# Optimization experiments

Measured on AMD Instinct MI355X. Metric: run time of the kernel, lower is better.

The kernel has to match this reference:

```python
import jax, jax.numpy as jnp
import numpy as np

N_NODES = 50000
HEADS = 4
OUT_DIM = 64
NEG_SLOPE = 0.2
BETA = 0.5
C_CONST = 1.0
EPS = 1e-16


def setup_inputs() -> dict:
    key = jax.random.key(0)
    ks = jax.random.split(key, 6)
    in_dim = 128
    x = jax.random.normal(ks[0], (N_NODES, in_dim), dtype=jnp.float32)
    edge_index = jax.random.randint(ks[1], (2, 800000), 0, N_NODES, dtype=jnp.int64)
    # GATConv params (glorot-ish scale)
    W = jax.random.normal(ks[2], (in_dim, HEADS * OUT_DIM), dtype=jnp.float32) * (1.0 / np.sqrt(in_dim))
    att_src = jax.random.normal(ks[3], (HEADS, OUT_DIM), dtype=jnp.float32) * (1.0 / np.sqrt(OUT_DIM))
    att_dst = jax.random.normal(ks[4], (HEADS, OUT_DIM), dtype=jnp.float32) * (1.0 / np.sqrt(OUT_DIM))
    bias = jnp.zeros((HEADS * OUT_DIM,), dtype=jnp.float32)
    return {"x": x, "edge_index": edge_index, "W": W, "att_src": att_src,
            "att_dst": att_dst, "bias": bias}


def _gat_conv(x, edge_index, W, att_src, att_dst, bias):
    N = x.shape[0]
    # add self loops (PyG GATConv default)
    loop = jnp.arange(N, dtype=edge_index.dtype)
    src = jnp.concatenate([edge_index[0], loop])
    dst = jnp.concatenate([edge_index[1], loop])
    # linear transform: [N, H, F]
    h = (x @ W).reshape(N, HEADS, OUT_DIM)
    # per-node attention logits: [N, H]
    a_src = jnp.einsum('nhf,hf->nh', h, att_src)
    a_dst = jnp.einsum('nhf,hf->nh', h, att_dst)
    # per-edge logits and segment softmax over destination nodes
    e = jax.nn.leaky_relu(a_src[src] + a_dst[dst], negative_slope=NEG_SLOPE)  # [E, H]
    m = jax.ops.segment_max(e, dst, num_segments=N)                           # [N, H]
    ex = jnp.exp(e - m[dst])
    s = jax.ops.segment_sum(ex, dst, num_segments=N)                          # [N, H]
    alpha = ex / (s[dst] + EPS)                                               # [E, H]
    # aggregate messages: [N, H, F]
    out = jax.ops.segment_sum(alpha[:, :, None] * h[src], dst, num_segments=N)
    return out.reshape(N, HEADS * OUT_DIM) + bias


def reference(x, edge_index, W, att_src, att_dst, bias):
    # eval mode: feature dropout and attention dropout are identity
    z = _gat_conv(x, edge_index, W, att_src, att_dst, bias)
    return BETA * z + (C_CONST - BETA) * jax.nn.elu(z)
```

## Files before the change

kernel.cpp:

```cpp
#include <hip/hip_runtime.h>
#include <hip/hip_bf16.h>

typedef unsigned short u16;
typedef __attribute__((ext_vector_type(8))) short bf16x8;
typedef __attribute__((ext_vector_type(4))) float f32x4;

#define HEADS 4
#define OUT_DIM 64
#define HF 256
#define IN_DIM 128
#define NEG_SLOPE 0.2f
#define EPSF 1e-16f

__device__ __forceinline__ float braw2f(u16 u) {
    union { float f; unsigned int i; } c; c.i = ((unsigned int)u) << 16; return c.f;
}
__device__ __forceinline__ u16 f2braw(float v) {
    __hip_bfloat16 t = __float2bfloat16(v);
    return *(u16*)&t;
}
__device__ __forceinline__ float lrelu(float e) { return e < 0.f ? NEG_SLOPE * e : e; }

__device__ __forceinline__ bool detect_i64(const int* ei) {
    return (ei[1] | ei[3] | ei[5] | ei[7] | ei[9] | ei[11] | ei[13] | ei[15]) == 0;
}
__device__ __forceinline__ void get_edge(const int* ei, int E, int t, bool i64,
                                         int& s, int& d) {
    if (t < E) {
        if (i64) { s = ei[2 * t]; d = ei[2 * (E + t)]; }
        else     { s = ei[t];     d = ei[E + t]; }
    } else {
        s = d = t - E;
    }
}

__global__ __launch_bounds__(256) void init_kernel(const float* __restrict__ W,
                                                   const float* __restrict__ att_s,
                                                   const float* __restrict__ att_d,
                                                   float* __restrict__ wa_s,
                                                   float* __restrict__ wa_d,
                                                   int* __restrict__ cnt,
                                                   int* __restrict__ cur,
                                                   int* __restrict__ gcnt,
                                                   int* __restrict__ hist,
                                                   int* __restrict__ bcur,
                                                   int N, int NZ) {
    int b = blockIdx.x;
    if (b == 0) {
        if (threadIdx.x == 0) *gcnt = 0;
        hist[threadIdx.x] = 0;
        bcur[threadIdx.x] = 0;
    }
    if (b < NZ) {
        int i = b * 256 + threadIdx.x;
        if (i < N) { cnt[i] = 0; cur[i] = 0; }
    } else {
        for (int idx = threadIdx.x; idx < HEADS * IN_DIM; idx += 256) {
            int h = idx >> 7, k = idx & 127;
            float ss = 0.f, sd = 0.f;
            for (int f = 0; f < OUT_DIM; ++f) {
                float wv = W[k * HF + h * OUT_DIM + f];
                ss = fmaf(wv, att_s[h * OUT_DIM + f], ss);
                sd = fmaf(wv, att_d[h * OUT_DIM + f], sd);
            }
            wa_s[idx] = ss;
            wa_d[idx] = sd;
        }
    }
}

__global__ __launch_bounds__(256) void phase1_kernel(const float* __restrict__ x,
                                                     const int* __restrict__ ei,
                                                     const float* __restrict__ W,
                                                     const float* __restrict__ wa_s,
                                                     const float* __restrict__ wa_d,
                                                     float* __restrict__ a_src,
                                                     float* __restrict__ a_dst,
                                                     u16* __restrict__ xb,
                                                     u16* __restrict__ Wfrag,
                                                     int* __restrict__ cnt,
                                                     int N, int E, int NA, int NC) {
    int b = blockIdx.x;
    if (b < NA) {
        int wid = threadIdx.x >> 6;
        int l = threadIdx.x & 63;
        int g = l >> 4, c = l & 15, kc = c * 8;
        int v = b * 16 + wid * 4 + g;
        if (v >= N) return;

        const float4* xr = (const float4*)(x + (size_t)v * IN_DIM + kc);
        float4 x0 = xr[0], x1 = xr[1];

        uint4 u;
        u.x = (unsigned)f2braw(x0.x) | ((unsigned)f2braw(x0.y) << 16);
        u.y = (unsigned)f2braw(x0.z) | ((unsigned)f2braw(x0.w) << 16);
        u.z = (unsigned)f2braw(x1.x) | ((unsigned)f2braw(x1.y) << 16);
        u.w = (unsigned)f2braw(x1.z) | ((unsigned)f2braw(x1.w) << 16);
        *(uint4*)(xb + (size_t)v * IN_DIM + kc) = u;

        float ps[4], pd[4];
        #pragma unroll
        for (int h = 0; h < 4; ++h) {
            const float4* s4 = (const float4*)(wa_s + h * IN_DIM + kc);
            const float4* d4 = (const float4*)(wa_d + h * IN_DIM + kc);
            float4 s0 = s4[0], s1 = s4[1], d0 = d4[0], d1 = d4[1];
            ps[h] = x0.x*s0.x + x0.y*s0.y + x0.z*s0.z + x0.w*s0.w
                  + x1.x*s1.x + x1.y*s1.y + x1.z*s1.z + x1.w*s1.w;
            pd[h] = x0.x*d0.x + x0.y*d0.y + x0.z*d0.z + x0.w*d0.w
                  + x1.x*d1.x + x1.y*d1.y + x1.z*d1.z + x1.w*d1.w;
        }
        #pragma unroll
        for (int off = 1; off < 16; off <<= 1) {
            #pragma unroll
            for (int h = 0; h < 4; ++h) {
                ps[h] += __shfl_xor(ps[h], off);
                pd[h] += __shfl_xor(pd[h], off);
            }
        }
        if (c == 0) {
            float4 vs, vd;
            vs.x = ps[0]; vs.y = ps[1]; vs.z = ps[2]; vs.w = ps[3];
            vd.x = pd[0]; vd.y = pd[1]; vd.z = pd[2]; vd.w = pd[3];
            *(float4*)(a_src + (size_t)v * HEADS) = vs;
            *(float4*)(a_dst + (size_t)v * HEADS) = vd;
        }
    } else if (b < NA + NC) {
        int t = (b - NA) * 256 + threadIdx.x;
        if (t >= E + N) return;
        bool i64 = detect_i64(ei);
        int src, dst; get_edge(ei, E, t, i64, src, dst);
        if (src >= 0 && src < N && dst >= 0 && dst < N) atomicAdd(cnt + dst, 1);
    } else {
        int bb = b - NA - NC;
        for (int idx = bb * 256 + threadIdx.x; idx < 32768; idx += 8 * 256) {
            int j = idx & 7, l = (idx >> 3) & 63, t = (idx >> 9) & 3;
            int s = (idx >> 11) & 3, h = (idx >> 13) & 3;
            int k = s * 32 + ((l >> 4) & 3) * 8 + j;
            int col = h * OUT_DIM + t * 16 + (l & 15);
            Wfrag[idx] = f2braw(W[k * HF + col]);
        }
    }
}

__global__ __launch_bounds__(256) void offset_kernel(const int* __restrict__ cnt,
                                                     int* __restrict__ offs,
                                                     int* __restrict__ gcnt,
                                                     int* __restrict__ hist, int N) {
    __shared__ int lh[256];
    lh[threadIdx.x] = 0;
    __syncthreads();

    int idx = blockIdx.x * 256 + threadIdx.x;
    int l = threadIdx.x & 63;
    int d = (idx < N) ? cnt[idx] : 0;
    if (idx < N) atomicAdd(lh + min(max(d, 0), 255), 1);

    int s = d;
    #pragma unroll
    for (int off = 1; off < 64; off <<= 1) {
        int t = __shfl_up(s, off);
        if (l >= off) s += t;
    }
    int base = 0;
    if (l == 63) base = atomicAdd(gcnt, s);
    base = __shfl(base, 63);
    if (idx < N) offs[idx] = base + s - d;

    __syncthreads();
    if (lh[threadIdx.x]) atomicAdd(hist + threadIdx.x, lh[threadIdx.x]);
}

__global__ __launch_bounds__(256) void bscan_kernel(const int* __restrict__ hist,
                                                    int* __restrict__ bbase, int N) {
    __shared__ int sc[256];
    int tid = threadIdx.x;
    sc[tid] = hist[tid];
    __syncthreads();
    #pragma unroll
    for (int off = 1; off < 256; off <<= 1) {
        int t = (tid >= off) ? sc[tid - off] : 0;
        __syncthreads();
        sc[tid] += t;
        __syncthreads();
    }
    bbase[tid] = N - sc[tid];
}

__global__ __launch_bounds__(256) void scatter_kernel(const int* __restrict__ cnt,
                                                      const int* __restrict__ bbase,
                                                      int* __restrict__ bcur,
                                                      int* __restrict__ perm, int N) {
    __shared__ int lh[256];
    __shared__ int lbase[256];
    lh[threadIdx.x] = 0;
    __syncthreads();

    int idx = blockIdx.x * 256 + threadIdx.x;
    int b = 0, mypos = 0;
    bool valid = (idx < N);
    if (valid) {
        b = min(max(cnt[idx], 0), 255);
        mypos = atomicAdd(lh + b, 1);
    }
    __syncthreads();
    int c = lh[threadIdx.x];
    if (c) lbase[threadIdx.x] = atomicAdd(bcur + threadIdx.x, c);
    __syncthreads();
    if (valid) {
        int p = bbase[b] + lbase[b] + mypos;
        if (p >= 0 && p < N) perm[p] = idx;
    }
}

__global__ __launch_bounds__(256) void fill_kernel(const int* __restrict__ ei,
                                                   const int* __restrict__ offs,
                                                   int* __restrict__ cur,
                                                   int* __restrict__ slots,
                                                   uint2* __restrict__ wslots,
                                                   const float* __restrict__ a_src,
                                                   const float* __restrict__ a_dst,
                                                   int E, int N) {
    int t = blockIdx.x * 256 + threadIdx.x;
    if (t >= E + N) return;
    bool i64 = detect_i64(ei);
    int src, dst; get_edge(ei, E, t, i64, src, dst);
    if (src >= 0 && src < N && dst >= 0 && dst < N) {
        int pos = atomicAdd(cur + dst, 1);
        int idx = offs[dst] + pos;
        slots[idx] = src;
        if (wslots) {
            float4 as = ((const float4*)a_src)[src];
            float4 ad = ((const float4*)a_dst)[dst];
            float w0 = __expf(lrelu(as.x + ad.x));
            float w1 = __expf(lrelu(as.y + ad.y));
            float w2 = __expf(lrelu(as.z + ad.z));
            float w3 = __expf(lrelu(as.w + ad.w));
            uint2 wp;
            wp.x = (unsigned)f2braw(w0) | ((unsigned)f2braw(w1) << 16);
            wp.y = (unsigned)f2braw(w2) | ((unsigned)f2braw(w3) << 16);
            wslots[idx] = wp;
        }
    }
}

#define ACC_EDGE(wp, r) do { \
    float w0_ = braw2f((wp).x & 0xffff), w1_ = braw2f((wp).x >> 16); \
    float w2_ = braw2f((wp).y & 0xffff), w3_ = braw2f((wp).y >> 16); \
    ls0 += w0_; ls1 += w1_; ls2 += w2_; ls3 += w3_; \
    float xv_[8]; \
    xv_[0] = braw2f((r).x & 0xffff); xv_[1] = braw2f((r).x >> 16); \
    xv_[2] = braw2f((r).y & 0xffff); xv_[3] = braw2f((r).y >> 16); \
    xv_[4] = braw2f((r).z & 0xffff); xv_[5] = braw2f((r).z >> 16); \
    xv_[6] = braw2f((r).w & 0xffff); xv_[7] = braw2f((r).w >> 16); \
    _Pragma("unroll") \
    for (int q_ = 0; q_ < 8; ++q_) { \
        G0[q_] = fmaf(w0_, xv_[q_], G0[q_]); \
        G1[q_] = fmaf(w1_, xv_[q_], G1[q_]); \
        G2[q_] = fmaf(w2_, xv_[q_], G2[q_]); \
        G3[q_] = fmaf(w3_, xv_[q_], G3[q_]); \
    } \
} while (0)

__global__ __launch_bounds__(512) void fused_gz_kernel(const int* __restrict__ perm,
                                                       const int* __restrict__ offs,
                                                       const int* __restrict__ cnt,
                                                       const int* __restrict__ slots,
                                                       const uint2* __restrict__ wslots,
                                                       const u16* __restrict__ xb,
                                                       const u16* __restrict__ Wfrag,
                                                       const float* __restrict__ bias,
                                                       float* __restrict__ out,
                                                       int N, int ET) {
    __shared__ u16 smem[32 * 520];
    __shared__ int pvals[32];

    int tid = threadIdx.x;
    int wid = tid >> 6;
    int l = tid & 63;
    int g = l >> 4, c = l & 15, kc = c * 8;
    int n = wid * 4 + g;
    int pidx = blockIdx.x * 32 + n;

    int v = -1;
    if (pidx < N) {
        v = perm[pidx];
        if (v < 0 || v >= N) v = -1;
    }
    if (c == 0) pvals[n] = v;

    int beg = 0, end = 0;
    if (v >= 0) {
        beg = offs[v];
        int deg = cnt[v];
        beg = max(0, min(beg, ET));
        end = max(beg, min(beg + deg, ET));
    }

    float ls0 = 0.f, ls1 = 0.f, ls2 = 0.f, ls3 = 0.f;
    float G0[8] = {0,0,0,0,0,0,0,0};
    float G1[8] = {0,0,0,0,0,0,0,0};
    float G2[8] = {0,0,0,0,0,0,0,0};
    float G3[8] = {0,0,0,0,0,0,0,0};

    int j = beg;
    for (; j + 4 <= end; j += 4) {
        int s0 = max(0, min(slots[j],     N - 1));
        int s1 = max(0, min(slots[j + 1], N - 1));
        int s2 = max(0, min(slots[j + 2], N - 1));
        int s3 = max(0, min(slots[j + 3], N - 1));
        uint2 wp0 = wslots[j];
        uint2 wp1 = wslots[j + 1];
        uint2 wp2 = wslots[j + 2];
        uint2 wp3 = wslots[j + 3];
        uint4 r0 = *(const uint4*)(xb + (size_t)s0 * IN_DIM + kc);
        uint4 r1 = *(const uint4*)(xb + (size_t)s1 * IN_DIM + kc);
        uint4 r2 = *(const uint4*)(xb + (size_t)s2 * IN_DIM + kc);
        uint4 r3 = *(const uint4*)(xb + (size_t)s3 * IN_DIM + kc);
        ACC_EDGE(wp0, r0);
        ACC_EDGE(wp1, r1);
        ACC_EDGE(wp2, r2);
        ACC_EDGE(wp3, r3);
    }
    for (; j < end; ++j) {
        int s0 = max(0, min(slots[j], N - 1));
        uint2 wp0 = wslots[j];
        uint4 r0 = *(const uint4*)(xb + (size_t)s0 * IN_DIM + kc);
        ACC_EDGE(wp0, r0);
    }

    if (v >= 0) {
        float i0 = 1.f / (ls0 + EPSF), i1 = 1.f / (ls1 + EPSF);
        float i2 = 1.f / (ls2 + EPSF), i3 = 1.f / (ls3 + EPSF);
        u16* lp = smem + n * 520 + c * 8;
        #pragma unroll
        for (int h = 0; h < 4; ++h) {
            const float* G = h == 0 ? G0 : h == 1 ? G1 : h == 2 ? G2 : G3;
            float inv = h == 0 ? i0 : h == 1 ? i1 : h == 2 ? i2 : i3;
            uint4 u;
            u.x = (unsigned)f2braw(G[0] * inv) | ((unsigned)f2braw(G[1] * inv) << 16);
            u.y = (unsigned)f2braw(G[2] * inv) | ((unsigned)f2braw(G[3] * inv) << 16);
            u.z = (unsigned)f2braw(G[4] * inv) | ((unsigned)f2braw(G[5] * inv) << 16);
            u.w = (unsigned)f2braw(G[6] * inv) | ((unsigned)f2braw(G[7] * inv) << 16);
            *(uint4*)(lp + h * 128) = u;
        }
    }
    __syncthreads();

    int t = wid >> 2;
    int h = wid & 3;
    int q = l >> 4, mcol = l & 15;

    const u16* lp = smem + (t * 16 + mcol) * 520 + h * 128 + q * 8;
    bf16x8 A[4];
    A[0] = *(const bf16x8*)(lp);
    A[1] = *(const bf16x8*)(lp + 32);
    A[2] = *(const bf16x8*)(lp + 64);
    A[3] = *(const bf16x8*)(lp + 96);

    f32x4 acc0 = {0.f,0.f,0.f,0.f}, acc1 = acc0, acc2 = acc0, acc3 = acc0;
    #pragma unroll
    for (int s = 0; s < 4; ++s) {
        const u16* wb = Wfrag + (((h * 4 + s) * 4) << 9) + l * 8;
        bf16x8 B0 = *(const bf16x8*)(wb);
        bf16x8 B1 = *(const bf16x8*)(wb + 512);
        bf16x8 B2 = *(const bf16x8*)(wb + 1024);
        bf16x8 B3 = *(const bf16x8*)(wb + 1536);
        acc0 = __builtin_amdgcn_mfma_f32_16x16x32_bf16(A[s], B0, acc0, 0, 0, 0);
        acc1 = __builtin_amdgcn_mfma_f32_16x16x32_bf16(A[s], B1, acc1, 0, 0, 0);
        acc2 = __builtin_amdgcn_mfma_f32_16x16x32_bf16(A[s], B2, acc2, 0, 0, 0);
        acc3 = __builtin_amdgcn_mfma_f32_16x16x32_bf16(A[s], B3, acc3, 0, 0, 0);
    }

    #pragma unroll
    for (int bt = 0; bt < 4; ++bt) {
        f32x4 a = bt == 0 ? acc0 : bt == 1 ? acc1 : bt == 2 ? acc2 : acc3;
        float b = bias[h * OUT_DIM + bt * 16 + mcol];
        #pragma unroll
        for (int r = 0; r < 4; ++r) {
            int vv = pvals[t * 16 + q * 4 + r];
            if (vv >= 0) {
                float z = a[r] + b;
                float y = z > 0.f ? z : 0.5f * z + 0.5f * (__expf(z) - 1.f);
                out[(size_t)vv * HF + h * OUT_DIM + bt * 16 + mcol] = y;
            }
        }
    }
}

__global__ __launch_bounds__(512) void gather_bf_kernel(const int* __restrict__ offs,
                                                        const int* __restrict__ cnt,
                                                        const int* __restrict__ slots,
                                                        const u16* __restrict__ xb,
                                                        const float* __restrict__ a_src,
                                                        const float* __restrict__ a_dst,
                                                        u16* __restrict__ Gout, int N, int ET) {
    int v = (blockIdx.x * 512 + threadIdx.x) >> 6;
    int l = threadIdx.x & 63;
    if (v >= N) return;
    int h = l >> 4, c = l & 15, kc = c * 8;

    int beg = offs[v];
    int deg = cnt[v];
    beg = max(0, min(beg, ET));
    int end = max(beg, min(beg + deg, ET));
    float adh = a_dst[v * HEADS + h];

    float ls = 0.f;
    float G[8] = {0.f,0.f,0.f,0.f,0.f,0.f,0.f,0.f};

    int j = beg;
    for (; j + 4 <= end; j += 4) {
        int s0 = max(0, min(slots[j],     N - 1));
        int s1 = max(0, min(slots[j + 1], N - 1));
        int s2 = max(0, min(slots[j + 2], N - 1));
        int s3 = max(0, min(slots[j + 3], N - 1));
        float w0 = __expf(lrelu(a_src[s0 * HEADS + h] + adh));
        float w1 = __expf(lrelu(a_src[s1 * HEADS + h] + adh));
        float w2 = __expf(lrelu(a_src[s2 * HEADS + h] + adh));
        float w3 = __expf(lrelu(a_src[s3 * HEADS + h] + adh));
        uint4 r0 = *(const uint4*)(xb + (size_t)s0 * IN_DIM + kc);
        uint4 r1 = *(const uint4*)(xb + (size_t)s1 * IN_DIM + kc);
        uint4 r2 = *(const uint4*)(xb + (size_t)s2 * IN_DIM + kc);
        uint4 r3 = *(const uint4*)(xb + (size_t)s3 * IN_DIM + kc);
        ls += (w0 + w1) + (w2 + w3);
        unsigned ua[4];
        ua[0]=r0.x; ua[1]=r0.y; ua[2]=r0.z; ua[3]=r0.w;
        #pragma unroll
        for (int q = 0; q < 4; ++q) {
            G[2*q]   = fmaf(w0, braw2f(ua[q] & 0xffff), G[2*q]);
            G[2*q+1] = fmaf(w0, braw2f(ua[q] >> 16),    G[2*q+1]);
        }
        ua[0]=r1.x; ua[1]=r1.y; ua[2]=r1.z; ua[3]=r1.w;
        #pragma unroll
        for (int q = 0; q < 4; ++q) {
            G[2*q]   = fmaf(w1, braw2f(ua[q] & 0xffff), G[2*q]);
            G[2*q+1] = fmaf(w1, braw2f(ua[q] >> 16),    G[2*q+1]);
        }
        ua[0]=r2.x; ua[1]=r2.y; ua[2]=r2.z; ua[3]=r2.w;
        #pragma unroll
        for (int q = 0; q < 4; ++q) {
            G[2*q]   = fmaf(w2, braw2f(ua[q] & 0xffff), G[2*q]);
            G[2*q+1] = fmaf(w2, braw2f(ua[q] >> 16),    G[2*q+1]);
        }
        ua[0]=r3.x; ua[1]=r3.y; ua[2]=r3.z; ua[3]=r3.w;
        #pragma unroll
        for (int q = 0; q < 4; ++q) {
            G[2*q]   = fmaf(w3, braw2f(ua[q] & 0xffff), G[2*q]);
            G[2*q+1] = fmaf(w3, braw2f(ua[q] >> 16),    G[2*q+1]);
        }
    }
    for (; j < end; ++j) {
        int s0 = max(0, min(slots[j], N - 1));
        float w0 = __expf(lrelu(a_src[s0 * HEADS + h] + adh));
        uint4 r0 = *(const uint4*)(xb + (size_t)s0 * IN_DIM + kc);
        ls += w0;
        unsigned ua[4]; ua[0]=r0.x; ua[1]=r0.y; ua[2]=r0.z; ua[3]=r0.w;
        #pragma unroll
        for (int q = 0; q < 4; ++q) {
            G[2*q]   = fmaf(w0, braw2f(ua[q] & 0xffff), G[2*q]);
            G[2*q+1] = fmaf(w0, braw2f(ua[q] >> 16),    G[2*q+1]);
        }
    }

    float inv = 1.f / (ls + EPSF);
    uint4 u;
    u.x = (unsigned)f2braw(G[0] * inv) | ((unsigned)f2braw(G[1] * inv) << 16);
    u.y = (unsigned)f2braw(G[2] * inv) | ((unsigned)f2braw(G[3] * inv) << 16);
    u.z = (unsigned)f2braw(G[4] * inv) | ((unsigned)f2braw(G[5] * inv) << 16);
    u.w = (unsigned)f2braw(G[6] * inv) | ((unsigned)f2braw(G[7] * inv) << 16);
    *(uint4*)(Gout + (size_t)v * 512 + h * 128 + kc) = u;
}

__global__ __launch_bounds__(512) void gather_f32_kernel(const int* __restrict__ offs,
                                                         const int* __restrict__ cnt,
                                                         const int* __restrict__ slots,
                                                         const float* __restrict__ x,
                                                         const float* __restrict__ a_src,
                                                         const float* __restrict__ a_dst,
                                                         u16* __restrict__ Gout, int N, int ET) {
    int v = (blockIdx.x * 512 + threadIdx.x) >> 6;
    int l = threadIdx.x & 63;
    if (v >= N) return;
    int h = l >> 4, c = l & 15, kc = c * 8;

    int beg = offs[v];
    int deg = cnt[v];
    beg = max(0, min(beg, ET));
    int end = max(beg, min(beg + deg, ET));
    float adh = a_dst[v * HEADS + h];

    float ls = 0.f;
    float G[8] = {0.f,0.f,0.f,0.f,0.f,0.f,0.f,0.f};
    for (int j = beg; j < end; ++j) {
        int s0 = max(0, min(slots[j], N - 1));
        float w0 = __expf(lrelu(a_src[s0 * HEADS + h] + adh));
        const float4* xr0 = (const float4*)(x + (size_t)s0 * IN_DIM + kc);
        float4 a0 = xr0[0], b0 = xr0[1];
        ls += w0;
        G[0]=fmaf(w0,a0.x,G[0]); G[1]=fmaf(w0,a0.y,G[1]);
        G[2]=fmaf(w0,a0.z,G[2]); G[3]=fmaf(w0,a0.w,G[3]);
        G[4]=fmaf(w0,b0.x,G[4]); G[5]=fmaf(w0,b0.y,G[5]);
        G[6]=fmaf(w0,b0.z,G[6]); G[7]=fmaf(w0,b0.w,G[7]);
    }
    float inv = 1.f / (ls + EPSF);
    uint4 u;
    u.x = (unsigned)f2braw(G[0] * inv) | ((unsigned)f2braw(G[1] * inv) << 16);
    u.y = (unsigned)f2braw(G[2] * inv) | ((unsigned)f2braw(G[3] * inv) << 16);
    u.z = (unsigned)f2braw(G[4] * inv) | ((unsigned)f2braw(G[5] * inv) << 16);
    u.w = (unsigned)f2braw(G[6] * inv) | ((unsigned)f2braw(G[7] * inv) << 16);
    *(uint4*)(Gout + (size_t)v * 512 + h * 128 + kc) = u;
}

__global__ __launch_bounds__(256) void zgemm_kernel(const u16* __restrict__ Wfrag,
                                                    const float* __restrict__ bias,
                                                    float* __restrict__ out, int N) {
    int h = threadIdx.x >> 6;
    int l = threadIdx.x & 63;
    int q = l >> 4, mcol = l & 15;
    int nb = blockIdx.x * 16;

    const u16* G = (const u16*)out;
    bool valid = (nb + mcol) < N;
    int vA = valid ? nb + mcol : N - 1;
    const u16* gp = G + (size_t)vA * 512 + h * 128 + q * 8;
    bf16x8 A[4];
    A[0] = *(const bf16x8*)(gp);
    A[1] = *(const bf16x8*)(gp + 32);
    A[2] = *(const bf16x8*)(gp + 64);
    A[3] = *(const bf16x8*)(gp + 96);
    if (!valid) {
        bf16x8 zz = {0,0,0,0,0,0,0,0};
        A[0] = zz; A[1] = zz; A[2] = zz; A[3] = zz;
    }

    f32x4 acc0 = {0.f,0.f,0.f,0.f}, acc1 = acc0, acc2 = acc0, acc3 = acc0;
    #pragma unroll
    for (int s = 0; s < 4; ++s) {
        const u16* wb = Wfrag + (((h * 4 + s) * 4) << 9) + l * 8;
        bf16x8 B0 = *(const bf16x8*)(wb);
        bf16x8 B1 = *(const bf16x8*)(wb + 512);
        bf16x8 B2 = *(const bf16x8*)(wb + 1024);
        bf16x8 B3 = *(const bf16x8*)(wb + 1536);
        acc0 = __builtin_amdgcn_mfma_f32_16x16x32_bf16(A[s], B0, acc0, 0, 0, 0);
        acc1 = __builtin_amdgcn_mfma_f32_16x16x32_bf16(A[s], B1, acc1, 0, 0, 0);
        acc2 = __builtin_amdgcn_mfma_f32_16x16x32_bf16(A[s], B2, acc2, 0, 0, 0);
        acc3 = __builtin_amdgcn_mfma_f32_16x16x32_bf16(A[s], B3, acc3, 0, 0, 0);
    }

    #pragma unroll
    for (int t = 0; t < 4; ++t) {
        f32x4 a = t == 0 ? acc0 : t == 1 ? acc1 : t == 2 ? acc2 : acc3;
        float b = bias[h * OUT_DIM + t * 16 + mcol];
        #pragma unroll
        for (int r = 0; r < 4; ++r) {
            int v = nb + q * 4 + r;
            if (v < N) {
                float z = a[r] + b;
                float y = z > 0.f ? z : 0.5f * z + 0.5f * (__expf(z) - 1.f);
                out[(size_t)v * HF + h * OUT_DIM + t * 16 + mcol] = y;
            }
        }
    }
}

extern "C" void kernel_launch(void* const* d_in, const int* in_sizes, int n_in,
                              void* d_out, int out_size, void* d_ws, size_t ws_size,
                              hipStream_t stream) {
    const float* x       = (const float*)d_in[0];
    const int*   ei      = (const int*)d_in[1];
    const float* W       = (const float*)d_in[2];
    const float* att_src = (const float*)d_in[3];
    const float* att_dst = (const float*)d_in[4];
    const float* bias    = (const float*)d_in[5];

    const int N = in_sizes[0] / IN_DIM;
    const int E = in_sizes[1] / 2;
    const int ET = E + N;
    const int NT = (N + 255) / 256;

    char* ws = (char*)d_ws;
    size_t off = 0;
    float* wa_s   = (float*)(ws + off); off += HEADS * IN_DIM * 4;
    float* wa_d   = (float*)(ws + off); off += HEADS * IN_DIM * 4;
    u16*   Wfrag  = (u16*)(ws + off);   off += 32768 * 2;
    float* a_src  = (float*)(ws + off); off += (size_t)N * HEADS * 4;
    float* a_dst  = (float*)(ws + off); off += (size_t)N * HEADS * 4;
    int*   offs   = (int*)(ws + off);   off += ((size_t)N * 4 + 15) & ~(size_t)15;
    int*   cnt    = (int*)(ws + off);   off += ((size_t)N * 4 + 15) & ~(size_t)15;
    int*   cur    = (int*)(ws + off);   off += ((size_t)N * 4 + 15) & ~(size_t)15;
    int*   gcnt   = (int*)(ws + off);   off += 64;
    int*   hist   = (int*)(ws + off);   off += 256 * 4;
    int*   bbase  = (int*)(ws + off);   off += 256 * 4;
    int*   bcur   = (int*)(ws + off);   off += 256 * 4;
    int*   perm   = (int*)(ws + off);   off += ((size_t)N * 4 + 15) & ~(size_t)15;
    int*   slots  = (int*)(ws + off);   off += ((size_t)ET * 4 + 15) & ~(size_t)15;
    u16*   xb     = (u16*)(ws + off);   size_t need_bf = off + (size_t)N * IN_DIM * 2;
    uint2* wslots = (uint2*)(ws + need_bf);
    size_t need_w = need_bf + (size_t)ET * 8;
    bool use_bf = (ws_size >= need_bf);
    bool use_w  = (ws_size >= need_w);

    const int NA = (N + 15) / 16;
    const int NC = (ET + 255) / 256;

    init_kernel<<<NT + 1, 256, 0, stream>>>(W, att_src, att_dst, wa_s, wa_d,
                                            cnt, cur, gcnt, hist, bcur, N, NT);
    phase1_kernel<<<NA + NC + 8, 256, 0, stream>>>(x, ei, W, wa_s, wa_d, a_src, a_dst,
                                                   use_bf ? xb : (u16*)d_out,
                                                   Wfrag, cnt, N, E, NA, NC);
    offset_kernel<<<NT, 256, 0, stream>>>(cnt, offs, gcnt, hist, N);
    fill_kernel<<<(ET + 255) / 256, 256, 0, stream>>>(ei, offs, cur, slots,
                                                      use_w ? wslots : (uint2*)0,
                                                      a_src, a_dst, E, N);
    if (use_w) {
        bscan_kernel<<<1, 256, 0, stream>>>(hist, bbase, N);
        scatter_kernel<<<NT, 256, 0, stream>>>(cnt, bbase, bcur, perm, N);
        fused_gz_kernel<<<(N + 31) / 32, 512, 0, stream>>>(perm, offs, cnt, slots,
                                                           wslots, xb, Wfrag, bias,
                                                           (float*)d_out, N, ET);
    } else if (use_bf) {
        gather_bf_kernel<<<(N * 64 + 511) / 512, 512, 0, stream>>>(offs, cnt, slots, xb,
                                                                   a_src, a_dst,
                                                                   (u16*)d_out, N, ET);
        zgemm_kernel<<<(N + 15) / 16, 256, 0, stream>>>(Wfrag, bias, (float*)d_out, N);
    } else {
        gather_f32_kernel<<<(N * 64 + 511) / 512, 512, 0, stream>>>(offs, cnt, slots, x,
                                                                    a_src, a_dst,
                                                                    (u16*)d_out, N, ET);
        zgemm_kernel<<<(N + 15) / 16, 256, 0, stream>>>(Wfrag, bias, (float*)d_out, N);
    }
}
```

Measured before the change: 255.6 us.

## Merge fill, bucket scan and scatter into one launch; prefetch edge slots in gather

```diff
diff --git a/kernel.cpp b/kernel.cpp
--- a/kernel.cpp
+++ b/kernel.cpp
@@ -170,75 +170,72 @@
     if (lh[threadIdx.x]) atomicAdd(hist + threadIdx.x, lh[threadIdx.x]);
 }
 
-__global__ __launch_bounds__(256) void bscan_kernel(const int* __restrict__ hist,
-                                                    int* __restrict__ bbase, int N) {
+__global__ __launch_bounds__(256) void fillscatter_kernel(const int* __restrict__ ei,
+                                                          const int* __restrict__ offs,
+                                                          int* __restrict__ cur,
+                                                          int* __restrict__ slots,
+                                                          uint2* __restrict__ wslots,
+                                                          const float* __restrict__ a_src,
+                                                          const float* __restrict__ a_dst,
+                                                          const int* __restrict__ cnt,
+                                                          const int* __restrict__ hist,
+                                                          int* __restrict__ bcur,
+                                                          int* __restrict__ perm,
+                                                          int E, int N, int NC) {
     __shared__ int sc[256];
-    int tid = threadIdx.x;
-    sc[tid] = hist[tid];
-    __syncthreads();
-    #pragma unroll
-    for (int off = 1; off < 256; off <<= 1) {
-        int t = (tid >= off) ? sc[tid - off] : 0;
-        __syncthreads();
-        sc[tid] += t;
-        __syncthreads();
-    }
-    bbase[tid] = N - sc[tid];
-}
-
-__global__ __launch_bounds__(256) void scatter_kernel(const int* __restrict__ cnt,
-                                                      const int* __restrict__ bbase,
-                                                      int* __restrict__ bcur,
-                                                      int* __restrict__ perm, int N) {
     __shared__ int lh[256];
     __shared__ int lbase[256];
-    lh[threadIdx.x] = 0;
-    __syncthreads();
-
-    int idx = blockIdx.x * 256 + threadIdx.x;
-    int b = 0, mypos = 0;
-    bool valid = (idx < N);
-    if (valid) {
-        b = min(max(cnt[idx], 0), 255);
-        mypos = atomicAdd(lh + b, 1);
-    }
-    __syncthreads();
-    int c = lh[threadIdx.x];
-    if (c) lbase[threadIdx.x] = atomicAdd(bcur + threadIdx.x, c);
-    __syncthreads();
-    if (valid) {
-        int p = bbase[b] + lbase[b] + mypos;
-        if (p >= 0 && p < N) perm[p] = idx;
-    }
-}
-
-__global__ __launch_bounds__(256) void fill_kernel(const int* __restrict__ ei,
-                                                   const int* __restrict__ offs,
-                                                   int* __restrict__ cur,
-                                                   int* __restrict__ slots,
-                                                   uint2* __restrict__ wslots,
-                                                   const float* __restrict__ a_src,
-                                                   const float* __restrict__ a_dst,
-                                                   int E, int N) {
-    int t = blockIdx.x * 256 + threadIdx.x;
-    if (t >= E + N) return;
-    bool i64 = detect_i64(ei);
-    int src, dst; get_edge(ei, E, t, i64, src, dst);
-    if (src >= 0 && src < N && dst >= 0 && dst < N) {
-        int pos = atomicAdd(cur + dst, 1);
-        int idx = offs[dst] + pos;
-        slots[idx] = src;
-        if (wslots) {
-            float4 as = ((const float4*)a_src)[src];
-            float4 ad = ((const float4*)a_dst)[dst];
-            float w0 = __expf(lrelu(as.x + ad.x));
-            float w1 = __expf(lrelu(as.y + ad.y));
-            float w2 = __expf(lrelu(as.z + ad.z));
-            float w3 = __expf(lrelu(as.w + ad.w));
-            uint2 wp;
-            wp.x = (unsigned)f2braw(w0) | ((unsigned)f2braw(w1) << 16);
-            wp.y = (unsigned)f2braw(w2) | ((unsigned)f2braw(w3) << 16);
-            wslots[idx] = wp;
+
+    int b = blockIdx.x;
+    if (b < NC) {
+        int t = b * 256 + threadIdx.x;
+        if (t >= E + N) return;
+        bool i64 = detect_i64(ei);
+        int src, dst; get_edge(ei, E, t, i64, src, dst);
+        if (src >= 0 && src < N && dst >= 0 && dst < N) {
+            int pos = atomicAdd(cur + dst, 1);
+            int idx = offs[dst] + pos;
+            slots[idx] = src;
+            if (wslots) {
+                float4 as = ((const float4*)a_src)[src];
+                float4 ad = ((const float4*)a_dst)[dst];
+                float w0 = __expf(lrelu(as.x + ad.x));
+                float w1 = __expf(lrelu(as.y + ad.y));
+                float w2 = __expf(lrelu(as.z + ad.z));
+                float w3 = __expf(lrelu(as.w + ad.w));
+                uint2 wp;
+                wp.x = (unsigned)f2braw(w0) | ((unsigned)f2braw(w1) << 16);
+                wp.y = (unsigned)f2braw(w2) | ((unsigned)f2braw(w3) << 16);
+                wslots[idx] = wp;
+            }
+        }
+    } else {
+        int tid = threadIdx.x;
+        sc[tid] = hist[tid];
+        lh[tid] = 0;
+        __syncthreads();
+        #pragma unroll
+        for (int off = 1; off < 256; off <<= 1) {
+            int tv = (tid >= off) ? sc[tid - off] : 0;
+            __syncthreads();
+            sc[tid] += tv;
+            __syncthreads();
+        }
+
+        int idx = (b - NC) * 256 + tid;
+        int bk = 0, mypos = 0;
+        bool valid = (idx < N);
+        if (valid) {
+            bk = min(max(cnt[idx], 0), 255);
+            mypos = atomicAdd(lh + bk, 1);
+        }
+        __syncthreads();
+        int c = lh[tid];
+        if (c) lbase[tid] = atomicAdd(bcur + tid, c);
+        __syncthreads();
+        if (valid) {
+            int p = (N - sc[bk]) + lbase[bk] + mypos;
+            if (p >= 0 && p < N) perm[p] = idx;
         }
     }
 }
@@ -303,26 +300,43 @@
     float G3[8] = {0,0,0,0,0,0,0,0};
 
     int j = beg;
-    for (; j + 4 <= end; j += 4) {
-        int s0 = max(0, min(slots[j],     N - 1));
-        int s1 = max(0, min(slots[j + 1], N - 1));
-        int s2 = max(0, min(slots[j + 2], N - 1));
-        int s3 = max(0, min(slots[j + 3], N - 1));
-        uint2 wp0 = wslots[j];
-        uint2 wp1 = wslots[j + 1];
-        uint2 wp2 = wslots[j + 2];
-        uint2 wp3 = wslots[j + 3];
+    int sn0 = 0, sn1 = 0, sn2 = 0, sn3 = 0;
+    uint2 wn0 = {0,0}, wn1 = {0,0}, wn2 = {0,0}, wn3 = {0,0};
+    if (j + 4 <= end) {
+        sn0 = slots[j];     sn1 = slots[j + 1];
+        sn2 = slots[j + 2]; sn3 = slots[j + 3];
+        wn0 = wslots[j];     wn1 = wslots[j + 1];
+        wn2 = wslots[j + 2]; wn3 = wslots[j + 3];
+    }
+    for (; j + 8 <= end; j += 4) {
+        int s0 = sn0, s1 = sn1, s2 = sn2, s3 = sn3;
+        uint2 wp0 = wn0, wp1 = wn1, wp2 = wn2, wp3 = wn3;
         uint4 r0 = *(const uint4*)(xb + (size_t)s0 * IN_DIM + kc);
         uint4 r1 = *(const uint4*)(xb + (size_t)s1 * IN_DIM + kc);
         uint4 r2 = *(const uint4*)(xb + (size_t)s2 * IN_DIM + kc);
         uint4 r3 = *(const uint4*)(xb + (size_t)s3 * IN_DIM + kc);
+        sn0 = slots[j + 4]; sn1 = slots[j + 5];
+        sn2 = slots[j + 6]; sn3 = slots[j + 7];
+        wn0 = wslots[j + 4]; wn1 = wslots[j + 5];
+        wn2 = wslots[j + 6]; wn3 = wslots[j + 7];
         ACC_EDGE(wp0, r0);
         ACC_EDGE(wp1, r1);
         ACC_EDGE(wp2, r2);
         ACC_EDGE(wp3, r3);
     }
+    if (j + 4 <= end) {
+        uint4 r0 = *(const uint4*)(xb + (size_t)sn0 * IN_DIM + kc);
+        uint4 r1 = *(const uint4*)(xb + (size_t)sn1 * IN_DIM + kc);
+        uint4 r2 = *(const uint4*)(xb + (size_t)sn2 * IN_DIM + kc);
+        uint4 r3 = *(const uint4*)(xb + (size_t)sn3 * IN_DIM + kc);
+        ACC_EDGE(wn0, r0);
+        ACC_EDGE(wn1, r1);
+        ACC_EDGE(wn2, r2);
+        ACC_EDGE(wn3, r3);
+        j += 4;
+    }
     for (; j < end; ++j) {
-        int s0 = max(0, min(slots[j], N - 1));
+        int s0 = slots[j];
         uint2 wp0 = wslots[j];
         uint4 r0 = *(const uint4*)(xb + (size_t)s0 * IN_DIM + kc);
         ACC_EDGE(wp0, r0);
@@ -590,7 +604,7 @@
     int*   cur    = (int*)(ws + off);   off += ((size_t)N * 4 + 15) & ~(size_t)15;
     int*   gcnt   = (int*)(ws + off);   off += 64;
     int*   hist   = (int*)(ws + off);   off += 256 * 4;
-    int*   bbase  = (int*)(ws + off);   off += 256 * 4;
+    off += 256 * 4;
     int*   bcur   = (int*)(ws + off);   off += 256 * 4;
     int*   perm   = (int*)(ws + off);   off += ((size_t)N * 4 + 15) & ~(size_t)15;
     int*   slots  = (int*)(ws + off);   off += ((size_t)ET * 4 + 15) & ~(size_t)15;
@@ -609,12 +623,10 @@
                                                    use_bf ? xb : (u16*)d_out,
                                                    Wfrag, cnt, N, E, NA, NC);
     offset_kernel<<<NT, 256, 0, stream>>>(cnt, offs, gcnt, hist, N);
-    fill_kernel<<<(ET + 255) / 256, 256, 0, stream>>>(ei, offs, cur, slots,
-                                                      use_w ? wslots : (uint2*)0,
-                                                      a_src, a_dst, E, N);
+    fillscatter_kernel<<<NC + (use_w ? NT : 0), 256, 0, stream>>>(
+        ei, offs, cur, slots, use_w ? wslots : (uint2*)0, a_src, a_dst,
+        cnt, hist, bcur, perm, E, N, NC);
     if (use_w) {
-        bscan_kernel<<<1, 256, 0, stream>>>(hist, bbase, N);
-        scatter_kernel<<<NT, 256, 0, stream>>>(cnt, bbase, bcur, perm, N);
         fused_gz_kernel<<<(N + 31) / 32, 512, 0, stream>>>(perm, offs, cnt, slots,
                                                            wslots, xb, Wfrag, bias,
                                                            (float*)d_out, N, ET);
```

Result: slower. 265.4 us (+3.8%).
